# Kernel optimization log

Hardware: AMD Instinct MI355X
Metric: run time of the kernel (lower is better)

Reference implementation:

```python
import jax, jax.numpy as jnp
import numpy as np

B = 65536          # batch
N_IN = 256         # input nodes (topology level 0)
G = 16             # node groups per level (joined nodes with shared dependency set)
U = 16             # units (joined nodes) per group -> 256 nodes per level
F = 32             # fan-in (input_node_coords) per group
LEVELS = 4


def setup_inputs() -> dict:
    key = jax.random.key(0)
    ks = jax.random.split(key, 13)
    inp = {"x": jax.random.normal(ks[0], (B, N_IN), dtype=jnp.float32)}
    for l in range(LEVELS):
        inp[f"k{l+1}"] = jax.random.normal(ks[1 + 3 * l], (G, F, U), dtype=jnp.float32) * 0.2
        inp[f"b{l+1}"] = jax.random.normal(ks[2 + 3 * l], (G, U), dtype=jnp.float32) * 0.1
        # flat coords into concatenation of all prior level outputs (levels 0..l)
        hi = N_IN + l * (G * U)
        inp[f"idx{l+1}"] = jax.random.randint(ks[3 + 3 * l], (G, F), 0, hi, dtype=jnp.int32)
    return inp


def reference(x, k1, b1, k2, b2, k3, b3, k4, b4, idx1, idx2, idx3, idx4):
    kernels = [k1, k2, k3, k4]
    biases = [b1, b2, b3, b4]
    idxs = [idx1, idx2, idx3, idx4]
    # `flat` is the column-wise concatenation of all prior topology-level outputs
    # (equivalent to the `inputs` list of per-level tensors in the original model,
    # with (layer_index, node_index) coords flattened to a single column index).
    flat = x
    out = x
    for K, b, idx in zip(kernels, biases, idxs):
        sel = flat[:, idx]                                   # gather: [B, G, F]
        out = jnp.tanh(jnp.einsum('bgf,gfu->bgu', sel, K) + b)  # tiny matmul+bias+act
        out = out.reshape(out.shape[0], G * U)               # per-level concat of groups
        flat = jnp.concatenate([flat, out], axis=1)
    return out  # last level output, [B, G*U]
```

## Files before the change

kernel.cpp:

```cpp
#include <hip/hip_runtime.h>
#include <stdint.h>

#define NIN 256
#define RPB 32

typedef float    f32x4 __attribute__((ext_vector_type(4)));
typedef _Float16 half8 __attribute__((ext_vector_type(8)));
typedef __fp16   fp16x2 __attribute__((ext_vector_type(2)));
typedef uint32_t u32x4 __attribute__((ext_vector_type(4)));

#define SEL_LO 0x05040100u
#define SEL_HI 0x07060302u

static __device__ __forceinline__ float fast_tanh(float x) {
    float e = __builtin_amdgcn_exp2f(x * 2.8853900817779268f);
    return 1.0f - 2.0f * __builtin_amdgcn_rcpf(e + 1.0f);
}
static __device__ __forceinline__ unsigned pkrtz(float a, float b) {
    fp16x2 h = __builtin_amdgcn_cvt_pkrtz(a, b);
    return __builtin_bit_cast(unsigned, h);
}

extern "C" __global__ void kprep_kernel(const float* __restrict__ k1, const float* __restrict__ k2,
                                        const float* __restrict__ k3, const float* __restrict__ k4,
                                        const int* __restrict__ i1, const int* __restrict__ i2,
                                        const int* __restrict__ i3, const int* __restrict__ i4,
                                        uint32_t* __restrict__ kt, int* __restrict__ apre) {
    const int bx  = blockIdx.x;
    const int lvl = bx >> 2;
    const float* Kp = (lvl == 0) ? k1 : (lvl == 1) ? k2 : (lvl == 2) ? k3 : k4;
    const int*   Ip = (lvl == 0) ? i1 : (lvl == 1) ? i2 : (lvl == 2) ? i3 : i4;
    const int sub = (bx & 3) * 256 + threadIdx.x;
    const int g = sub >> 6, q = (sub >> 4) & 3, n = sub & 15;
    const float* src = Kp + (size_t)(g * 32 + q * 8) * 16 + n;
    const float v0 = src[0],  v1 = src[16], v2 = src[32], v3 = src[48];
    const float v4 = src[64], v5 = src[80], v6 = src[96], v7 = src[112];
    u32x4 pk;
    pk.x = pkrtz(v0, v1); pk.y = pkrtz(v2, v3);
    pk.z = pkrtz(v4, v5); pk.w = pkrtz(v6, v7);
    *(u32x4*)(kt + (size_t)(lvl * 1024 + sub) * 4) = pk;

    if ((bx & 3) < 2) {
        const int f = (bx & 3) * 256 + threadIdx.x;
        const int col = Ip[f];
        apre[lvl * 512 + f] = (col << 6) ^ (((col >> 1) & 3) << 4);
    }
}


extern "C" __global__ __launch_bounds__(1024, 8)
void denc_kernel(const float* __restrict__ x,
                 const int* __restrict__ a1, const float* __restrict__ b1,
                 const int* __restrict__ a2, const float* __restrict__ b2,
                 const int* __restrict__ a3, const float* __restrict__ b3,
                 const int* __restrict__ a4, const float* __restrict__ b4,
                 const uint32_t* __restrict__ kt,
                 float* __restrict__ out)
{
    __shared__ int4 ftile[4096];
    const char* tfc = (const char*)ftile;

    const int tid  = threadIdx.x;
    const int w    = tid >> 6;
    const int lane = tid & 63;
    const int q    = lane >> 4;
    const int n    = lane & 15;
    const int R0   = blockIdx.x * RPB;
    const int Ln   = n << 2;

    {
        const int c = tid & 255;
        const int j = tid >> 8;
        const float* xb = x + (size_t)R0 * 256 + c;
        uint32_t qp[4];
        #pragma unroll
        for (int k = 0; k < 4; ++k) {
            const int p = j * 4 + k;
            qp[k] = pkrtz(xb[(size_t)p * 256], xb[(size_t)(p + 16) * 256]);
        }
        const int s = (c >> 1) & 3;
        ftile[c * 4 + (j ^ s)] = make_int4((int)qp[0], (int)qp[1], (int)qp[2], (int)qp[3]);
    }

    int4 pa = *(const int4*)(a1 + w * 32 + q * 8);
    int4 pb = *(const int4*)(a1 + w * 32 + q * 8 + 4);

#define LEVEL(ApNext, Bp, LVLBASE, OB, LAST) do { \
    __syncthreads(); \
    const uint32_t r0 = *(const uint32_t*)(tfc + (pa.x ^ Ln)); \
    const uint32_t r1 = *(const uint32_t*)(tfc + (pa.y ^ Ln)); \
    const uint32_t r2 = *(const uint32_t*)(tfc + (pa.z ^ Ln)); \
    const uint32_t r3 = *(const uint32_t*)(tfc + (pa.w ^ Ln)); \
    const uint32_t r4 = *(const uint32_t*)(tfc + (pb.x ^ Ln)); \
    const uint32_t r5 = *(const uint32_t*)(tfc + (pb.y ^ Ln)); \
    const uint32_t r6 = *(const uint32_t*)(tfc + (pb.z ^ Ln)); \
    const uint32_t r7 = *(const uint32_t*)(tfc + (pb.w ^ Ln)); \
    if (!(LAST)) {                                    \
        pa = *(const int4*)((ApNext) + w * 32 + q * 8); \
        pb = *(const int4*)((ApNext) + w * 32 + q * 8 + 4); \
    } \
    const u32x4 bf = *(const u32x4*)(kt + (size_t)((LVLBASE) + w * 64 + q * 16 + n) * 4); \
    const float bvv = (Bp)[w * 16 + n]; \
    f32x4 accA = {bvv, bvv, bvv, bvv}, accB = accA; \
    u32x4 fA, fB; \
    fA.x = __builtin_amdgcn_perm(r1, r0, SEL_LO); fB.x = __builtin_amdgcn_perm(r1, r0, SEL_HI); \
    fA.y = __builtin_amdgcn_perm(r3, r2, SEL_LO); fB.y = __builtin_amdgcn_perm(r3, r2, SEL_HI); \
    fA.z = __builtin_amdgcn_perm(r5, r4, SEL_LO); fB.z = __builtin_amdgcn_perm(r5, r4, SEL_HI); \
    fA.w = __builtin_amdgcn_perm(r7, r6, SEL_LO); fB.w = __builtin_amdgcn_perm(r7, r6, SEL_HI); \
    accA = __builtin_amdgcn_mfma_f32_16x16x32_f16( \
        __builtin_bit_cast(half8, fA), __builtin_bit_cast(half8, bf), accA, 0, 0, 0); \
    accB = __builtin_amdgcn_mfma_f32_16x16x32_f16( \
        __builtin_bit_cast(half8, fB), __builtin_bit_cast(half8, bf), accB, 0, 0, 0); \
    const float tA0 = fast_tanh(accA[0]), tA1 = fast_tanh(accA[1]); \
    const float tA2 = fast_tanh(accA[2]), tA3 = fast_tanh(accA[3]); \
    const float tB0 = fast_tanh(accB[0]), tB1 = fast_tanh(accB[1]); \
    const float tB2 = fast_tanh(accB[2]), tB3 = fast_tanh(accB[3]); \
    if (LAST) { \
        float* ob = out + (size_t)(R0 + q * 4) * 256 + w * 16 + n; \
        ob[0]    = tA0; ob[256]  = tA1; ob[512]  = tA2; ob[768]  = tA3; \
        ob[4096] = tB0; ob[4352] = tB1; ob[4608] = tB2; ob[4864] = tB3; \
    } else { \
        const int col = (OB) + w * 16 + n; \
        const int s = (col >> 1) & 3; \
        ftile[col * 4 + (q ^ s)] = make_int4( \
            (int)pkrtz(tA0, tB0), (int)pkrtz(tA1, tB1), \
            (int)pkrtz(tA2, tB2), (int)pkrtz(tA3, tB3)); \
    } \
} while (0)

    LEVEL(a2, b1,    0, NIN,       0);
    LEVEL(a3, b2, 1024, NIN + 256, 0);
    LEVEL(a4, b3, 2048, NIN + 512, 0);
    LEVEL(a4, b4, 3072, 0,         1);

#undef LEVEL
}

extern "C" void kernel_launch(void* const* d_in, const int* in_sizes, int n_in,
                              void* d_out, int out_size, void* d_ws, size_t ws_size,
                              hipStream_t stream) {
    const float* x  = (const float*)d_in[0];
    const float* k1 = (const float*)d_in[1];
    const float* b1 = (const float*)d_in[2];
    const int*   i1 = (const int*)  d_in[3];
    const float* k2 = (const float*)d_in[4];
    const float* b2 = (const float*)d_in[5];
    const int*   i2 = (const int*)  d_in[6];
    const float* k3 = (const float*)d_in[7];
    const float* b3 = (const float*)d_in[8];
    const int*   i3 = (const int*)  d_in[9];
    const float* k4 = (const float*)d_in[10];
    const float* b4 = (const float*)d_in[11];
    const int*   i4 = (const int*)  d_in[12];
    float* out = (float*)d_out;
    uint32_t* kt = (uint32_t*)d_ws;
    int* apre = (int*)((char*)d_ws + 65536);

    hipLaunchKernelGGL(kprep_kernel, dim3(16), dim3(256), 0, stream,
                       k1, k2, k3, k4, i1, i2, i3, i4, kt, apre);

    const int batch = in_sizes[0] / NIN;
    hipLaunchKernelGGL(denc_kernel, dim3(batch / RPB), dim3(1024), 0, stream,
                       x, apre, b1, apre + 512, b2, apre + 1024, b3, apre + 1536, b4,
                       (const uint32_t*)kt, out);
}
```

Baseline: 40.83 us.

## Process multiple row chunks per block, hoisting weights and biases into registers

Each block now handles four 32-row chunks in a loop instead of one, with the grid shrunk to match. The fp16 weight fragments and biases for all four levels are loaded into registers once per block rather than once per level per block. The next chunk's x tile is staged into shared memory after the last level's gather, before its compute and store. This cuts the block count from 2048 to 512, which amortizes the per-block weight loads and launch overhead but lowers parallelism, adds register pressure, and serializes the x loads inside each block.

```diff
diff --git a/kernel.cpp b/kernel.cpp
--- a/kernel.cpp
+++ b/kernel.cpp
@@ -3,6 +3,7 @@
 
 #define NIN 256
 #define RPB 32
+#define CHUNKS 4
 
 typedef float    f32x4 __attribute__((ext_vector_type(4)));
 typedef _Float16 half8 __attribute__((ext_vector_type(8)));
@@ -65,28 +66,32 @@
     const int lane = tid & 63;
     const int q    = lane >> 4;
     const int n    = lane & 15;
-    const int R0   = blockIdx.x * RPB;
     const int Ln   = n << 2;
+    const int R0b  = blockIdx.x * (RPB * CHUNKS);
 
-    {
-        const int c = tid & 255;
-        const int j = tid >> 8;
-        const float* xb = x + (size_t)R0 * 256 + c;
-        uint32_t qp[4];
-        #pragma unroll
-        for (int k = 0; k < 4; ++k) {
-            const int p = j * 4 + k;
-            qp[k] = pkrtz(xb[(size_t)p * 256], xb[(size_t)(p + 16) * 256]);
-        }
-        const int s = (c >> 1) & 3;
-        ftile[c * 4 + (j ^ s)] = make_int4((int)qp[0], (int)qp[1], (int)qp[2], (int)qp[3]);
-    }
+    const int ki = w * 64 + q * 16 + n;
+    const u32x4 bf1 = *(const u32x4*)(kt + (size_t)(ki)        * 4);
+    const u32x4 bf2 = *(const u32x4*)(kt + (size_t)(1024 + ki) * 4);
+    const u32x4 bf3 = *(const u32x4*)(kt + (size_t)(2048 + ki) * 4);
+    const u32x4 bf4 = *(const u32x4*)(kt + (size_t)(3072 + ki) * 4);
+    const float bv1 = b1[w * 16 + n], bv2 = b2[w * 16 + n];
+    const float bv3 = b3[w * 16 + n], bv4 = b4[w * 16 + n];
 
-    int4 pa = *(const int4*)(a1 + w * 32 + q * 8);
-    int4 pb = *(const int4*)(a1 + w * 32 + q * 8 + 4);
+#define STAGE(R0S) do { \
+    const int c = tid & 255; \
+    const int j = tid >> 8;                       \
+    const float* xb = x + (size_t)(R0S) * 256 + c; \
+    uint32_t qp0 = pkrtz(xb[(size_t)(j*4+0) * 256], xb[(size_t)(j*4+16) * 256]); \
+    uint32_t qp1 = pkrtz(xb[(size_t)(j*4+1) * 256], xb[(size_t)(j*4+17) * 256]); \
+    uint32_t qp2 = pkrtz(xb[(size_t)(j*4+2) * 256], xb[(size_t)(j*4+18) * 256]); \
+    uint32_t qp3 = pkrtz(xb[(size_t)(j*4+3) * 256], xb[(size_t)(j*4+19) * 256]); \
+    const int s = (c >> 1) & 3; \
+    ftile[c * 4 + (j ^ s)] = make_int4((int)qp0, (int)qp1, (int)qp2, (int)qp3); \
+} while (0)
 
-#define LEVEL(ApNext, Bp, LVLBASE, OB, LAST) do { \
-    __syncthreads(); \
+#define GATHER(Ap) \
+    const int4 pa = *(const int4*)((Ap) + w * 32 + q * 8); \
+    const int4 pb = *(const int4*)((Ap) + w * 32 + q * 8 + 4); \
     const uint32_t r0 = *(const uint32_t*)(tfc + (pa.x ^ Ln)); \
     const uint32_t r1 = *(const uint32_t*)(tfc + (pa.y ^ Ln)); \
     const uint32_t r2 = *(const uint32_t*)(tfc + (pa.z ^ Ln)); \
@@ -94,13 +99,11 @@
     const uint32_t r4 = *(const uint32_t*)(tfc + (pb.x ^ Ln)); \
     const uint32_t r5 = *(const uint32_t*)(tfc + (pb.y ^ Ln)); \
     const uint32_t r6 = *(const uint32_t*)(tfc + (pb.z ^ Ln)); \
-    const uint32_t r7 = *(const uint32_t*)(tfc + (pb.w ^ Ln)); \
-    if (!(LAST)) {                                    \
-        pa = *(const int4*)((ApNext) + w * 32 + q * 8); \
-        pb = *(const int4*)((ApNext) + w * 32 + q * 8 + 4); \
-    } \
-    const u32x4 bf = *(const u32x4*)(kt + (size_t)((LVLBASE) + w * 64 + q * 16 + n) * 4); \
-    const float bvv = (Bp)[w * 16 + n]; \
+    const uint32_t r7 = *(const uint32_t*)(tfc + (pb.w ^ Ln));
+
+#define COMPSTORE(BF, BV, OB, LAST) do { \
+    const u32x4 bf = (BF); \
+    const float bvv = (BV); \
     f32x4 accA = {bvv, bvv, bvv, bvv}, accB = accA; \
     u32x4 fA, fB; \
     fA.x = __builtin_amdgcn_perm(r1, r0, SEL_LO); fB.x = __builtin_amdgcn_perm(r1, r0, SEL_HI); \
@@ -128,12 +131,38 @@
     } \
 } while (0)
 
-    LEVEL(a2, b1,    0, NIN,       0);
-    LEVEL(a3, b2, 1024, NIN + 256, 0);
-    LEVEL(a4, b3, 2048, NIN + 512, 0);
-    LEVEL(a4, b4, 3072, 0,         1);
+    STAGE(R0b);
 
-#undef LEVEL
+    #pragma unroll 1
+    for (int ch = 0; ch < CHUNKS; ++ch) {
+        const int R0 = R0b + ch * RPB;
+        {
+            __syncthreads();
+            GATHER(a1)
+            COMPSTORE(bf1, bv1, NIN, 0);
+        }
+        {
+            __syncthreads();
+            GATHER(a2)
+            COMPSTORE(bf2, bv2, NIN + 256, 0);
+        }
+        {
+            __syncthreads();
+            GATHER(a3)
+            COMPSTORE(bf3, bv3, NIN + 512, 0);
+        }
+        {
+            __syncthreads();
+            GATHER(a4)
+            __syncthreads();
+            if (ch < CHUNKS - 1) STAGE(R0 + RPB);
+            COMPSTORE(bf4, bv4, 0, 1);
+        }
+    }
+
+#undef COMPSTORE
+#undef GATHER
+#undef STAGE
 }
 
 extern "C" void kernel_launch(void* const* d_in, const int* in_sizes, int n_in,
@@ -160,7 +189,7 @@
                        k1, k2, k3, k4, i1, i2, i3, i4, kt, apre);
 
     const int batch = in_sizes[0] / NIN;
-    hipLaunchKernelGGL(denc_kernel, dim3(batch / RPB), dim3(1024), 0, stream,
+    hipLaunchKernelGGL(denc_kernel, dim3(batch / (RPB * CHUNKS)), dim3(1024), 0, stream,
                        x, apre, b1, apre + 512, b2, apre + 1024, b3, apre + 1536, b4,
                        (const uint32_t*)kt, out);
 }
```

Result: slower. 90.38 us (+121.3%).
